# Performance work log

Hardware: AMD Instinct MI355X
Metric: run time of the kernel (lower is better)

The kernel has to match this reference:

```python
import jax, jax.numpy as jnp
import numpy as np

B, C, N, T = 16, 32, 1024, 64
C_OUT = 32
ORDER = 2
SMOOTH_DEPTH = 1


def setup_inputs() -> dict:
    key = jax.random.key(0)
    k1, k2, k3, k4 = jax.random.split(key, 4)
    x = jax.random.normal(k1, (B, C, N, T), dtype=jnp.float32)
    # row-normalized dense adjacencies (transition matrices), as used in Graph-WaveNet-style supports
    AL = jax.random.uniform(k2, (N, N), dtype=jnp.float32)
    AL = AL / AL.sum(axis=-1, keepdims=True)
    AS_pos = jax.random.uniform(k3, (N, N), dtype=jnp.float32)
    AS_pos = AS_pos / AS_pos.sum(axis=-1, keepdims=True)
    # 1x1 conv mlp: in_channels = (order*support_len+1)*c_in = 3*C, out_channels = C_OUT
    W_mlp = jax.random.normal(k4, (C_OUT, (ORDER + 1) * C), dtype=jnp.float32) * 0.02
    b_mlp = jnp.zeros((C_OUT,), dtype=jnp.float32)
    return {"x": x, "AL": AL, "AS_pos": AS_pos, "W_mlp": W_mlp, "b_mlp": b_mlp}


def reference(x, AL, AS_pos, W_mlp, b_mlp):
    # gcn_module.forward with short_bool=True, smooth_depth=SMOOTH_DEPTH, eval mode (no dropout)
    ALp = jnp.linalg.matrix_power(AL, SMOOTH_DEPTH)          # [N,N]
    # torch.einsum('bckj,ik->bcij', x, ALp): contract node dim of x against ALp
    x_long = jnp.einsum('ik,bckt->bcit', ALp, x)             # [B,C,N,T]
    x_short = x - x_long
    outs = [x]
    for _ in range(ORDER):
        # dnconv: einsum('nvw,ncwl->ncvl', A, x) with 2D A broadcast over batch
        x_long = jnp.einsum('vw,bcwt->bcvt', AL, x_long)
        x_short = jnp.einsum('vw,bcwt->bcvt', AS_pos, x_short)
        outs.append(x_long + x_short)
    h = jnp.concatenate(outs, axis=1)                        # [B,(ORDER+1)*C,N,T]
    # 1x1 conv == channel mixing
    h = jnp.einsum('oc,bcnt->bont', W_mlp, h) + b_mlp[None, :, None, None]
    return h
```

## Files before the change

### kernel.cpp

```cpp
#include <hip/hip_runtime.h>


typedef __bf16 bf16x8 __attribute__((ext_vector_type(8)));
typedef float f32x4 __attribute__((ext_vector_type(4)));
typedef unsigned int u32x4 __attribute__((ext_vector_type(4)));
typedef unsigned int u32x2 __attribute__((ext_vector_type(2)));

__device__ __forceinline__ unsigned short f2bf(float f) {
  unsigned u = __builtin_bit_cast(unsigned, f);
  u += 0x7fffu + ((u >> 16) & 1u);
  return (unsigned short)(u >> 16);
}
__device__ __forceinline__ float bf2f(unsigned short h) {
  unsigned u = ((unsigned)h) << 16;
  return __builtin_bit_cast(float, u);
}

static constexpr size_t OFF_YC    = 0;
static constexpr size_t OFF_ALBF  = 201326592;
static constexpr size_t OFF_ALT   = OFF_ALBF  + 2097152;
static constexpr size_t OFF_ASBF  = OFF_ALT   + 2097152;
static constexpr size_t OFF_AST   = OFF_ASBF  + 2097152;
static constexpr size_t OFF_AL2   = OFF_AST   + 2097152;
static constexpr size_t OFF_AL2T  = OFF_AL2   + 2097152;
static constexpr size_t OFF_ASAL  = OFF_AL2T  + 2097152;
static constexpr size_t OFF_AS2   = OFF_ASAL  + 2097152;
static constexpr size_t OFF_AL3   = OFF_AS2   + 2097152;
static constexpr size_t OFF_AS2AL = OFF_AL3   + 2097152;
static constexpr size_t OFF_G     = OFF_AS2AL + 2097152;

__global__ __launch_bounds__(256) void k_cast_bf16(const float* __restrict__ src,
                                                   unsigned short* __restrict__ dst,
                                                   int n4) {
  int i = blockIdx.x * 256 + threadIdx.x;
  if (i < n4) {
    float4 v = *((const float4*)src + i);
    unsigned lo = (unsigned)f2bf(v.x) | ((unsigned)f2bf(v.y) << 16);
    unsigned hi = (unsigned)f2bf(v.z) | ((unsigned)f2bf(v.w) << 16);
    u32x2 pk = {lo, hi};
    *(u32x2*)(dst + (size_t)i * 4) = pk;
  }
}

__global__ __launch_bounds__(256) void k_cast_wall(const float* __restrict__ W,
                                                   unsigned short* __restrict__ Wall) {
  int i = blockIdx.x * 256 + threadIdx.x;
  if (i < 3072) {
    int oo = i >> 5, c = i & 31;
    int o = oo & 31, g = oo >> 5;
    Wall[i] = f2bf(W[o * 96 + g * 32 + c]);
  }
}

__global__ __launch_bounds__(256) void k_transpose_cast(const float* __restrict__ src,
                                                        unsigned short* __restrict__ dst,
                                                        int R, int Cc) {
  __shared__ float Xs[64][65];
  const int tid = threadIdx.x;
  const size_t slice = (size_t)blockIdx.z * (size_t)R * (size_t)Cc;
  const float* s = src + slice;
  unsigned short* d = dst + slice;
  const int r0 = blockIdx.x * 64, c0 = blockIdx.y * 64;
  const int lrow = tid >> 4, lc4 = tid & 15;
#pragma unroll
  for (int rr = 0; rr < 4; rr++) {
    int row = rr * 16 + lrow;
    float4 v = *(const float4*)(s + (size_t)(r0 + row) * Cc + c0 + lc4 * 4);
    Xs[row][lc4 * 4 + 0] = v.x;
    Xs[row][lc4 * 4 + 1] = v.y;
    Xs[row][lc4 * 4 + 2] = v.z;
    Xs[row][lc4 * 4 + 3] = v.w;
  }
  __syncthreads();
  const int wc = tid & 7;
#pragma unroll
  for (int u = 0; u < 2; u++) {
    int t = u * 32 + (tid >> 3);
    unsigned v0 = (unsigned)f2bf(Xs[wc * 8 + 0][t]) | ((unsigned)f2bf(Xs[wc * 8 + 1][t]) << 16);
    unsigned v1 = (unsigned)f2bf(Xs[wc * 8 + 2][t]) | ((unsigned)f2bf(Xs[wc * 8 + 3][t]) << 16);
    unsigned v2 = (unsigned)f2bf(Xs[wc * 8 + 4][t]) | ((unsigned)f2bf(Xs[wc * 8 + 5][t]) << 16);
    unsigned v3 = (unsigned)f2bf(Xs[wc * 8 + 6][t]) | ((unsigned)f2bf(Xs[wc * 8 + 7][t]) << 16);
    u32x4 pk = {v0, v1, v2, v3};
    *(u32x4*)(d + (size_t)(c0 + t) * R + r0 + wc * 8) = pk;
  }
}

__device__ __forceinline__ void gemm128_bt(const unsigned short* __restrict__ A,
                                           const unsigned short* __restrict__ Bt,
                                           unsigned short* __restrict__ Cp,
                                           int K, size_t ldc, int m0, int n0) {
  __shared__ unsigned short As[128 * 32];
  __shared__ unsigned short Bs[128 * 32];
  const int tid = threadIdx.x;
  const int wave = tid >> 6, lane = tid & 63;
  const int lane15 = lane & 15, quad = lane >> 4;
  const int wm = wave & 1, wn = wave >> 1;
  const int srow = lane >> 2;
  const int schunk = (lane & 3) * 8;

  const unsigned short* gA0 = A + (size_t)(m0 + wave * 16 + srow) * K + schunk;
  const unsigned short* gA1 = A + (size_t)(m0 + 64 + wave * 16 + srow) * K + schunk;
  const unsigned short* gB0 = Bt + (size_t)(n0 + wave * 16 + srow) * K + schunk;
  const unsigned short* gB1 = Bt + (size_t)(n0 + 64 + wave * 16 + srow) * K + schunk;
  unsigned short* lA0 = As + (wave * 16) * 32;
  unsigned short* lA1 = As + (64 + wave * 16) * 32;
  unsigned short* lB0 = Bs + (wave * 16) * 32;
  unsigned short* lB1 = Bs + (64 + wave * 16) * 32;

  f32x4 acc[4][4];
#pragma unroll
  for (int i = 0; i < 4; i++)
#pragma unroll
    for (int j = 0; j < 4; j++) acc[i][j] = (f32x4){0.f, 0.f, 0.f, 0.f};

  const unsigned short* pa = As + (wm * 64 + lane15) * 32 + quad * 8;
  const unsigned short* pb = Bs + (wn * 64 + lane15) * 32 + quad * 8;

  for (int kb = 0; kb < K; kb += 32) {
    __syncthreads();
    __builtin_amdgcn_global_load_lds(
        (const __attribute__((address_space(1))) unsigned int*)(gA0 + kb),
        (__attribute__((address_space(3))) unsigned int*)lA0, 16, 0, 0);
    __builtin_amdgcn_global_load_lds(
        (const __attribute__((address_space(1))) unsigned int*)(gA1 + kb),
        (__attribute__((address_space(3))) unsigned int*)lA1, 16, 0, 0);
    __builtin_amdgcn_global_load_lds(
        (const __attribute__((address_space(1))) unsigned int*)(gB0 + kb),
        (__attribute__((address_space(3))) unsigned int*)lB0, 16, 0, 0);
    __builtin_amdgcn_global_load_lds(
        (const __attribute__((address_space(1))) unsigned int*)(gB1 + kb),
        (__attribute__((address_space(3))) unsigned int*)lB1, 16, 0, 0);
    __syncthreads();

    bf16x8 av[4], bv[4];
#pragma unroll
    for (int mt = 0; mt < 4; mt++) av[mt] = *(const bf16x8*)(pa + mt * 16 * 32);
#pragma unroll
    for (int nt = 0; nt < 4; nt++) bv[nt] = *(const bf16x8*)(pb + nt * 16 * 32);
#pragma unroll
    for (int mt = 0; mt < 4; mt++)
#pragma unroll
      for (int nt = 0; nt < 4; nt++)
        acc[mt][nt] = __builtin_amdgcn_mfma_f32_16x16x32_bf16(av[mt], bv[nt], acc[mt][nt], 0, 0, 0);
  }

#pragma unroll
  for (int mt = 0; mt < 4; mt++) {
#pragma unroll
    for (int nt = 0; nt < 4; nt++) {
      const int col = n0 + wn * 64 + nt * 16 + lane15;
#pragma unroll
      for (int r = 0; r < 4; r++) {
        const int row = m0 + wm * 64 + mt * 16 + quad * 4 + r;
        Cp[(size_t)row * ldc + col] = f2bf(acc[mt][nt][r]);
      }
    }
  }
}

__global__ __launch_bounds__(256) void k_gemm_pre(char* ws, int stage) {
  const unsigned short* A;
  const unsigned short* Bt;
  unsigned short* Cp;
  const int z = blockIdx.z;
  unsigned short* ALbf = (unsigned short*)(ws + OFF_ALBF);
  unsigned short* ALt  = (unsigned short*)(ws + OFF_ALT);
  unsigned short* ASbf = (unsigned short*)(ws + OFF_ASBF);
  unsigned short* ASt  = (unsigned short*)(ws + OFF_AST);
  unsigned short* AL2  = (unsigned short*)(ws + OFF_AL2);
  unsigned short* ASAL = (unsigned short*)(ws + OFF_ASAL);
  unsigned short* AS2  = (unsigned short*)(ws + OFF_AS2);
  unsigned short* AL3  = (unsigned short*)(ws + OFF_AL3);
  unsigned short* AS2AL= (unsigned short*)(ws + OFF_AS2AL);
  if (stage == 0) {
    if (z == 0)      { A = ALbf; Bt = ALt;  Cp = AL2;  }
    else if (z == 1) { A = ASbf; Bt = ALt;  Cp = ASAL; }
    else             { A = ASbf; Bt = ASt;  Cp = AS2;  }
  } else {
    if (z == 0)      { A = AL2;  Bt = ALt;  Cp = AL3;  }
    else             { A = AS2;  Bt = ALt;  Cp = AS2AL;}
  }
  gemm128_bt(A, Bt, Cp, 1024, 1024, blockIdx.y * 128, blockIdx.x * 128);
}

__global__ __launch_bounds__(256) void k_assemble_G(const unsigned short* __restrict__ AL2,
                                                    const unsigned short* __restrict__ ASAL,
                                                    const float* __restrict__ ASf,
                                                    const unsigned short* __restrict__ AL3,
                                                    const unsigned short* __restrict__ AS2,
                                                    const unsigned short* __restrict__ AS2AL,
                                                    unsigned short* __restrict__ G) {
  int i = blockIdx.x * 256 + threadIdx.x;
  int r = i >> 10, c = i & 1023;
  float g1 = bf2f(AL2[i]) + ASf[i] - bf2f(ASAL[i]);
  float g2 = bf2f(AL3[i]) + bf2f(AS2[i]) - bf2f(AS2AL[i]);
  G[(size_t)r * 2048 + c]        = f2bf(g1);
  G[(size_t)r * 2048 + 1024 + c] = f2bf(g2);
}

__global__ __launch_bounds__(256, 8) void k_mix_g(const float* __restrict__ x,
                                                  const unsigned short* __restrict__ Wall,
                                                  unsigned short* __restrict__ Yc) {
  const int tid = threadIdx.x;
  const int sid = (blockIdx.x & 7) * 256 + (blockIdx.x >> 3);
  const int b   = sid >> 7;
  const int n8g = sid & 127;
  const int nbase = n8g * 8;
  const int wave = tid >> 6, lane = tid & 63;
  const int lane15 = lane & 15, quad = lane >> 4;
  const int t = wave * 16 + lane15;

  bf16x8 afr[6];
#pragma unroll
  for (int ot = 0; ot < 6; ot++)
    afr[ot] = *(const bf16x8*)(Wall + (ot * 16 + lane15) * 32 + quad * 8);

  const float* xb = x + (size_t)b * 2097152 + (size_t)(quad * 8) * 65536 + t;

  bf16x8 bfr[8];
#pragma unroll
  for (int nl = 0; nl < 8; nl++) {
    const float* xp = xb + (size_t)(nbase + nl) * 64;
    unsigned u[4];
#pragma unroll
    for (int e = 0; e < 4; e++) {
      float a  = xp[(size_t)(2 * e) * 65536];
      float c2 = xp[(size_t)(2 * e + 1) * 65536];
      u[e] = (unsigned)f2bf(a) | ((unsigned)f2bf(c2) << 16);
    }
    u32x4 pk = {u[0], u[1], u[2], u[3]};
    bfr[nl] = __builtin_bit_cast(bf16x8, pk);
  }

#pragma unroll
  for (int ot = 0; ot < 6; ot++) {
    f32x4 acc[8];
    const f32x4 z = (f32x4){0.f, 0.f, 0.f, 0.f};
#pragma unroll
    for (int nl = 0; nl < 8; nl++)
      acc[nl] = __builtin_amdgcn_mfma_f32_16x16x32_bf16(afr[ot], bfr[nl], z, 0, 0, 0);
    const int og = ot >> 1;
    const int o  = (ot & 1) * 16 + quad * 4;
    const size_t plane = (size_t)(og * 128 + n8g) * 262144;
#pragma unroll
    for (int r = 0; r < 4; r++) {
      unsigned u0 = (unsigned)f2bf(acc[0][r]) | ((unsigned)f2bf(acc[1][r]) << 16);
      unsigned u1 = (unsigned)f2bf(acc[2][r]) | ((unsigned)f2bf(acc[3][r]) << 16);
      unsigned u2 = (unsigned)f2bf(acc[4][r]) | ((unsigned)f2bf(acc[5][r]) << 16);
      unsigned u3 = (unsigned)f2bf(acc[6][r]) | ((unsigned)f2bf(acc[7][r]) << 16);
      u32x4 pk = {u0, u1, u2, u3};
      size_t j = (size_t)(b * 32 + o + r) * 64 + t;
      *(u32x4*)(Yc + plane + j * 8) = pk;
    }
  }
}

__global__ __launch_bounds__(512) void k_gemm_main8(const unsigned short* __restrict__ A,
                                                    const unsigned short* __restrict__ Yc,
                                                    const float* __restrict__ bm,
                                                    float* __restrict__ out) {
  __shared__ unsigned short lds[65536];
  const int tid = threadIdx.x;
  const int wave = tid >> 6, lane = tid & 63;
  const int lane15 = lane & 15, quad = lane >> 4;
  const int wr = wave >> 2, wc = wave & 3;

  const int bid = blockIdx.x;
  const int swz = (bid & 7) * 64 + (bid >> 3);
  const int nx = swz >> 2, my = swz & 3;
  const int m0 = my * 256, n0 = nx * 256;

  const int srow = tid >> 3;
  const int cB   = (tid & 7) ^ (srow & 7);
  const int skc  = cB << 3;
  const int ldst0 = (tid & ~63) << 3;

#define STAGE_A(rowbase, ldsptr, ktile)                                                 \
  do {                                                                                  \
    const unsigned short* _g =                                                          \
        A + (size_t)((rowbase) + srow) * 2048 + (size_t)((ktile) * 64 + skc);           \
    __builtin_amdgcn_global_load_lds(                                                   \
        (const __attribute__((address_space(1))) unsigned int*)_g,                      \
        (__attribute__((address_space(3))) unsigned int*)((ldsptr) + ldst0), 16, 0, 0); \
    __builtin_amdgcn_global_load_lds(                                                   \
        (const __attribute__((address_space(1))) unsigned int*)(_g + 131072),           \
        (__attribute__((address_space(3))) unsigned int*)((ldsptr) + 4096 + ldst0),     \
        16, 0, 0);                                                                      \
  } while (0)

#define STAGE_B(rowbase, ldsptr, ktile)                                                 \
  do {                                                                                  \
    const unsigned short* _g = Yc + (size_t)(128 + (ktile) * 8 + cB) * 262144 +         \
                               (size_t)((rowbase) + srow) * 8;                          \
    __builtin_amdgcn_global_load_lds(                                                   \
        (const __attribute__((address_space(1))) unsigned int*)_g,                      \
        (__attribute__((address_space(3))) unsigned int*)((ldsptr) + ldst0), 16, 0, 0); \
    __builtin_amdgcn_global_load_lds(                                                   \
        (const __attribute__((address_space(1))) unsigned int*)(_g + 512),              \
        (__attribute__((address_space(3))) unsigned int*)((ldsptr) + 4096 + ldst0),     \
        16, 0, 0);                                                                      \
  } while (0)

#define LOAD_AFR(p)                                                                     \
  bf16x8 afr[2][2];                                                                     \
  _Pragma("unroll") for (int mi = 0; mi < 2; mi++)                                      \
      _Pragma("unroll") for (int kk = 0; kk < 2; kk++)                                  \
          afr[mi][kk] = *(const bf16x8*)(pA + (2 * (p) + mi) * 1024 + aks[kk]);

#define MFMA_QUAD(p)                                                                    \
  _Pragma("unroll") for (int kk = 0; kk < 2; kk++)                                      \
      _Pragma("unroll") for (int mi = 0; mi < 2; mi++)                                  \
          _Pragma("unroll") for (int n = 0; n < 4; n++)                                 \
              acc[2 * (p) + mi][n] = __builtin_amdgcn_mfma_f32_16x16x32_bf16(           \
                  afr[mi][kk], bfr[n][kk], acc[2 * (p) + mi][n], 0, 0, 0);

#define PHASE_SYNC_PRE()                              \
  asm volatile("" ::: "memory");                      \
  __builtin_amdgcn_s_barrier();                       \
  asm volatile("s_waitcnt lgkmcnt(0)" ::: "memory");  \
  __builtin_amdgcn_sched_barrier(0);                  \
  __builtin_amdgcn_s_setprio(1);

#define PHASE_SYNC_POST()                             \
  __builtin_amdgcn_s_setprio(0);                      \
  asm volatile("" ::: "memory");                      \
  __builtin_amdgcn_s_barrier();

  unsigned short* Acur = lds;
  unsigned short* Bcur = lds + 16384;
  unsigned short* Aalt = lds + 32768;
  unsigned short* Balt = lds + 49152;

  f32x4 acc[8][4];
#pragma unroll
  for (int i = 0; i < 8; i++)
#pragma unroll
    for (int j = 0; j < 4; j++) acc[i][j] = (f32x4){0.f, 0.f, 0.f, 0.f};

  const int swz8 = (lane15 & 7) << 3;
  int aks[2];
  aks[0] = (quad << 3) ^ swz8;
  aks[1] = (32 | (quad << 3)) ^ swz8;

  STAGE_B(n0,       Bcur,        0);
  STAGE_B(n0 + 128, Bcur + 8192, 0);
  STAGE_A(m0,       Acur,        0);
  STAGE_A(m0 + 128, Acur + 8192, 0);
  STAGE_B(n0,       Balt,        1);
  STAGE_B(n0 + 128, Balt + 8192, 1);
  STAGE_A(m0,       Aalt,        1);
  asm volatile("s_waitcnt vmcnt(6)" ::: "memory");
  __builtin_amdgcn_s_barrier();

  for (int u = 0; u < 30; ++u) {
    const unsigned short* pA = Acur + (wr * 128 + lane15) * 64;
    const unsigned short* pB = Bcur + (wc * 64 + lane15) * 64;
    bf16x8 bfr[4][2];
    {
#pragma unroll
      for (int n = 0; n < 4; n++)
#pragma unroll
        for (int kk = 0; kk < 2; kk++)
          bfr[n][kk] = *(const bf16x8*)(pB + n * 1024 + aks[kk]);
      LOAD_AFR(0)
      __builtin_amdgcn_sched_barrier(0);
      STAGE_A(m0 + 128, Aalt + 8192, u + 1);
      asm volatile("s_waitcnt lgkmcnt(8)" ::: "memory");
      PHASE_SYNC_PRE()
      MFMA_QUAD(0)
      PHASE_SYNC_POST()
    }
    {
      LOAD_AFR(1)
      __builtin_amdgcn_sched_barrier(0);
      STAGE_B(n0, Bcur, u + 2);
      PHASE_SYNC_PRE()
      MFMA_QUAD(1)
      PHASE_SYNC_POST()
    }
    {
      LOAD_AFR(2)
      __builtin_amdgcn_sched_barrier(0);
      STAGE_B(n0 + 128, Bcur + 8192, u + 2);
      PHASE_SYNC_PRE()
      MFMA_QUAD(2)
      PHASE_SYNC_POST()
    }
    {
      LOAD_AFR(3)
      __builtin_amdgcn_sched_barrier(0);
      STAGE_A(m0, Acur, u + 2);
      PHASE_SYNC_PRE()
      MFMA_QUAD(3)
      __builtin_amdgcn_s_setprio(0);
      asm volatile("s_waitcnt vmcnt(6)" ::: "memory");
      asm volatile("" ::: "memory");
      __builtin_amdgcn_s_barrier();
    }
    unsigned short* t;
    t = Acur; Acur = Aalt; Aalt = t;
    t = Bcur; Bcur = Balt; Balt = t;
  }

  {
    const unsigned short* pA = Acur + (wr * 128 + lane15) * 64;
    const unsigned short* pB = Bcur + (wc * 64 + lane15) * 64;
    bf16x8 bfr[4][2];
    {
#pragma unroll
      for (int n = 0; n < 4; n++)
#pragma unroll
        for (int kk = 0; kk < 2; kk++)
          bfr[n][kk] = *(const bf16x8*)(pB + n * 1024 + aks[kk]);
      LOAD_AFR(0)
      __builtin_amdgcn_sched_barrier(0);
      STAGE_A(m0 + 128, Aalt + 8192, 31);
      asm volatile("s_waitcnt lgkmcnt(8)" ::: "memory");
      PHASE_SYNC_PRE()
      MFMA_QUAD(0)
      PHASE_SYNC_POST()
    }
    { LOAD_AFR(1) PHASE_SYNC_PRE() MFMA_QUAD(1) PHASE_SYNC_POST() }
    { LOAD_AFR(2) PHASE_SYNC_PRE() MFMA_QUAD(2) PHASE_SYNC_POST() }
    {
      LOAD_AFR(3)
      PHASE_SYNC_PRE()
      MFMA_QUAD(3)
      __builtin_amdgcn_s_setprio(0);
      asm volatile("s_waitcnt vmcnt(0)" ::: "memory");
      asm volatile("" ::: "memory");
      __builtin_amdgcn_s_barrier();
    }
    unsigned short* t;
    t = Acur; Acur = Aalt; Aalt = t;
    t = Bcur; Bcur = Balt; Balt = t;
  }

  {
    const unsigned short* pA = Acur + (wr * 128 + lane15) * 64;
    const unsigned short* pB = Bcur + (wc * 64 + lane15) * 64;
    bf16x8 bfr[4][2];
#pragma unroll
    for (int n = 0; n < 4; n++)
#pragma unroll
      for (int kk = 0; kk < 2; kk++)
        bfr[n][kk] = *(const bf16x8*)(pB + n * 1024 + aks[kk]);
#pragma unroll
    for (int p = 0; p < 4; p++) {
      bf16x8 afr[2][2];
#pragma unroll
      for (int mi = 0; mi < 2; mi++)
#pragma unroll
        for (int kk = 0; kk < 2; kk++)
          afr[mi][kk] = *(const bf16x8*)(pA + (2 * p + mi) * 1024 + aks[kk]);
#pragma unroll
      for (int kk = 0; kk < 2; kk++)
#pragma unroll
        for (int mi = 0; mi < 2; mi++)
#pragma unroll
          for (int n = 0; n < 4; n++)
            acc[2 * p + mi][n] = __builtin_amdgcn_mfma_f32_16x16x32_bf16(
                afr[mi][kk], bfr[n][kk], acc[2 * p + mi][n], 0, 0, 0);
    }
  }

#pragma unroll
  for (int mt = 0; mt < 8; mt++) {
    const int row = m0 + wr * 128 + mt * 16 + quad * 4;
#pragma unroll
    for (int nf = 0; nf < 4; nf++) {
      const int col = n0 + wc * 64 + nf * 16 + lane15;
      const int bo_idx = col >> 6;
      const float bo = bm[bo_idx & 31];
      const size_t obase = (size_t)bo_idx * 65536 + (col & 63);
      ushort4 yv = *(const ushort4*)(Yc + (size_t)(row >> 3) * 262144 +
                                     (size_t)col * 8 + (row & 7));
      out[obase + (size_t)(row + 0) * 64] = acc[mt][nf][0] + bf2f(yv.x) + bo;
      out[obase + (size_t)(row + 1) * 64] = acc[mt][nf][1] + bf2f(yv.y) + bo;
      out[obase + (size_t)(row + 2) * 64] = acc[mt][nf][2] + bf2f(yv.z) + bo;
      out[obase + (size_t)(row + 3) * 64] = acc[mt][nf][3] + bf2f(yv.w) + bo;
    }
  }
#undef STAGE_A
#undef STAGE_B
#undef LOAD_AFR
#undef MFMA_QUAD
#undef PHASE_SYNC_PRE
#undef PHASE_SYNC_POST
}

extern "C" void kernel_launch(void* const* d_in, const int* in_sizes, int n_in,
                              void* d_out, int out_size, void* d_ws, size_t ws_size,
                              hipStream_t stream) {
  const float* x  = (const float*)d_in[0];
  const float* AL = (const float*)d_in[1];
  const float* AS = (const float*)d_in[2];
  const float* W  = (const float*)d_in[3];
  const float* bm = (const float*)d_in[4];
  float* out = (float*)d_out;
  char* ws = (char*)d_ws;

  unsigned short* Yc    = (unsigned short*)(ws + OFF_YC);
  unsigned short* ALbf  = (unsigned short*)(ws + OFF_ALBF);
  unsigned short* ALt   = (unsigned short*)(ws + OFF_ALT);
  unsigned short* ASbf  = (unsigned short*)(ws + OFF_ASBF);
  unsigned short* ASt   = (unsigned short*)(ws + OFF_AST);
  unsigned short* AL2   = (unsigned short*)(ws + OFF_AL2);
  unsigned short* ASAL  = (unsigned short*)(ws + OFF_ASAL);
  unsigned short* AS2   = (unsigned short*)(ws + OFF_AS2);
  unsigned short* AL3   = (unsigned short*)(ws + OFF_AL3);
  unsigned short* AS2AL = (unsigned short*)(ws + OFF_AS2AL);
  unsigned short* Gm    = (unsigned short*)(ws + OFF_G);
  unsigned short* Wall  = (unsigned short*)(ws + OFF_ALBF);

  k_cast_bf16<<<1024, 256, 0, stream>>>(AL, ALbf, 262144);
  k_cast_bf16<<<1024, 256, 0, stream>>>(AS, ASbf, 262144);
  k_transpose_cast<<<dim3(16, 16, 1), 256, 0, stream>>>(AL, ALt, 1024, 1024);
  k_transpose_cast<<<dim3(16, 16, 1), 256, 0, stream>>>(AS, ASt, 1024, 1024);
  k_gemm_pre<<<dim3(8, 8, 3), 256, 0, stream>>>(ws, 0);
  k_gemm_pre<<<dim3(8, 8, 2), 256, 0, stream>>>(ws, 1);
  k_assemble_G<<<4096, 256, 0, stream>>>(AL2, ASAL, AS, AL3, AS2, AS2AL, Gm);
  k_cast_wall<<<12, 256, 0, stream>>>(W, Wall);
  k_mix_g<<<2048, 256, 0, stream>>>(x, Wall, Yc);
  k_gemm_main8<<<dim3(512, 1, 1), 512, 0, stream>>>(Gm, Yc, bm, out);
}
```

Measured before the change: 519.1 us.

## Fuse adjacency prep kernels and re-pipeline main GEMM with ping-pong A fragments

The bf16 cast and transpose-cast of each adjacency become one k_prep kernel, which reads each source tile once and writes both layouts. The W cast is folded into block 0 of k_assemble_G, removing two launches. The main GEMM loop is restructured so that A fragments alternate between two register sets (afrP and afrQ): the next fragment's LDS reads and the async global-to-LDS stage are issued before a barrier, ahead of the current MFMA group. The loop-head barrier is moved and the vmcnt wait is loosened from 6 to 4. These changes aim to overlap LDS reads with MFMAs and reduce launch overhead, at the cost of more live registers and a subtler LDS hazard ordering.

```diff
diff --git a/kernel.cpp b/kernel.cpp
--- a/kernel.cpp
+++ b/kernel.cpp
@@ -29,47 +29,25 @@
 static constexpr size_t OFF_AS2AL = OFF_AL3   + 2097152;
 static constexpr size_t OFF_G     = OFF_AS2AL + 2097152;
 
-__global__ __launch_bounds__(256) void k_cast_bf16(const float* __restrict__ src,
-                                                   unsigned short* __restrict__ dst,
-                                                   int n4) {
-  int i = blockIdx.x * 256 + threadIdx.x;
-  if (i < n4) {
-    float4 v = *((const float4*)src + i);
-    unsigned lo = (unsigned)f2bf(v.x) | ((unsigned)f2bf(v.y) << 16);
-    unsigned hi = (unsigned)f2bf(v.z) | ((unsigned)f2bf(v.w) << 16);
-    u32x2 pk = {lo, hi};
-    *(u32x2*)(dst + (size_t)i * 4) = pk;
-  }
-}
-
-__global__ __launch_bounds__(256) void k_cast_wall(const float* __restrict__ W,
-                                                   unsigned short* __restrict__ Wall) {
-  int i = blockIdx.x * 256 + threadIdx.x;
-  if (i < 3072) {
-    int oo = i >> 5, c = i & 31;
-    int o = oo & 31, g = oo >> 5;
-    Wall[i] = f2bf(W[o * 96 + g * 32 + c]);
-  }
-}
-
-__global__ __launch_bounds__(256) void k_transpose_cast(const float* __restrict__ src,
-                                                        unsigned short* __restrict__ dst,
-                                                        int R, int Cc) {
+__global__ __launch_bounds__(256) void k_prep(const float* __restrict__ src,
+                                              unsigned short* __restrict__ dstN,
+                                              unsigned short* __restrict__ dstT) {
   __shared__ float Xs[64][65];
   const int tid = threadIdx.x;
-  const size_t slice = (size_t)blockIdx.z * (size_t)R * (size_t)Cc;
-  const float* s = src + slice;
-  unsigned short* d = dst + slice;
   const int r0 = blockIdx.x * 64, c0 = blockIdx.y * 64;
   const int lrow = tid >> 4, lc4 = tid & 15;
 #pragma unroll
   for (int rr = 0; rr < 4; rr++) {
     int row = rr * 16 + lrow;
-    float4 v = *(const float4*)(s + (size_t)(r0 + row) * Cc + c0 + lc4 * 4);
+    float4 v = *(const float4*)(src + (size_t)(r0 + row) * 1024 + c0 + lc4 * 4);
     Xs[row][lc4 * 4 + 0] = v.x;
     Xs[row][lc4 * 4 + 1] = v.y;
     Xs[row][lc4 * 4 + 2] = v.z;
     Xs[row][lc4 * 4 + 3] = v.w;
+    unsigned lo = (unsigned)f2bf(v.x) | ((unsigned)f2bf(v.y) << 16);
+    unsigned hi = (unsigned)f2bf(v.z) | ((unsigned)f2bf(v.w) << 16);
+    u32x2 pk = {lo, hi};
+    *(u32x2*)(dstN + (size_t)(r0 + row) * 1024 + c0 + lc4 * 4) = pk;
   }
   __syncthreads();
   const int wc = tid & 7;
@@ -81,7 +59,7 @@
     unsigned v2 = (unsigned)f2bf(Xs[wc * 8 + 4][t]) | ((unsigned)f2bf(Xs[wc * 8 + 5][t]) << 16);
     unsigned v3 = (unsigned)f2bf(Xs[wc * 8 + 6][t]) | ((unsigned)f2bf(Xs[wc * 8 + 7][t]) << 16);
     u32x4 pk = {v0, v1, v2, v3};
-    *(u32x4*)(d + (size_t)(c0 + t) * R + r0 + wc * 8) = pk;
+    *(u32x4*)(dstT + (size_t)(c0 + t) * 1024 + r0 + wc * 8) = pk;
   }
 }
 
@@ -189,7 +167,15 @@
                                                     const unsigned short* __restrict__ AL3,
                                                     const unsigned short* __restrict__ AS2,
                                                     const unsigned short* __restrict__ AS2AL,
+                                                    const float* __restrict__ W,
+                                                    unsigned short* __restrict__ Wall,
                                                     unsigned short* __restrict__ G) {
+  if (blockIdx.x == 0) {
+    for (int k = threadIdx.x; k < 3072; k += 256) {
+      int oo = k >> 5, c = k & 31;
+      Wall[k] = f2bf(W[(oo & 31) * 96 + (oo >> 5) * 32 + c]);
+    }
+  }
   int i = blockIdx.x * 256 + threadIdx.x;
   int r = i >> 10, c = i & 1023;
   float g1 = bf2f(AL2[i]) + ASf[i] - bf2f(ASAL[i]);
@@ -301,30 +287,31 @@
         16, 0, 0);                                                                      \
   } while (0)
 
-#define LOAD_AFR(p)                                                                     \
-  bf16x8 afr[2][2];                                                                     \
-  _Pragma("unroll") for (int mi = 0; mi < 2; mi++)                                      \
+#define RD_BFR()                                                                        \
+  _Pragma("unroll") for (int n = 0; n < 4; n++)                                         \
       _Pragma("unroll") for (int kk = 0; kk < 2; kk++)                                  \
-          afr[mi][kk] = *(const bf16x8*)(pA + (2 * (p) + mi) * 1024 + aks[kk]);
-
-#define MFMA_QUAD(p)                                                                    \
+          bfr[n][kk] = *(const bf16x8*)(pB + n * 1024 + aks[kk]);
+
+#define RD_AFR(FR, mA, mB)                                                              \
+  _Pragma("unroll") for (int kk = 0; kk < 2; kk++) {                                    \
+    FR[0][kk] = *(const bf16x8*)(pA + (mA) * 1024 + aks[kk]);                           \
+    FR[1][kk] = *(const bf16x8*)(pA + (mB) * 1024 + aks[kk]);                           \
+  }
+
+#define MFMA2(i0, FR)                                                                   \
   _Pragma("unroll") for (int kk = 0; kk < 2; kk++)                                      \
       _Pragma("unroll") for (int mi = 0; mi < 2; mi++)                                  \
           _Pragma("unroll") for (int n = 0; n < 4; n++)                                 \
-              acc[2 * (p) + mi][n] = __builtin_amdgcn_mfma_f32_16x16x32_bf16(           \
-                  afr[mi][kk], bfr[n][kk], acc[2 * (p) + mi][n], 0, 0, 0);
-
-#define PHASE_SYNC_PRE()                              \
-  asm volatile("" ::: "memory");                      \
-  __builtin_amdgcn_s_barrier();                       \
-  asm volatile("s_waitcnt lgkmcnt(0)" ::: "memory");  \
-  __builtin_amdgcn_sched_barrier(0);                  \
-  __builtin_amdgcn_s_setprio(1);
-
-#define PHASE_SYNC_POST()                             \
-  __builtin_amdgcn_s_setprio(0);                      \
-  asm volatile("" ::: "memory");                      \
+              acc[(i0) + mi][n] = __builtin_amdgcn_mfma_f32_16x16x32_bf16(              \
+                  FR[mi][kk], bfr[n][kk], acc[(i0) + mi][n], 0, 0, 0);
+
+#define SAFEBAR()                                                                       \
+  asm volatile("s_waitcnt lgkmcnt(0)" ::: "memory");                                    \
   __builtin_amdgcn_s_barrier();
+#define LGKM0() asm volatile("s_waitcnt lgkmcnt(0)" ::: "memory");                      \
+                __builtin_amdgcn_sched_barrier(0);
+#define PRIO1() __builtin_amdgcn_s_setprio(1);
+#define PRIO0() __builtin_amdgcn_s_setprio(0);
 
   unsigned short* Acur = lds;
   unsigned short* Bcur = lds + 16384;
@@ -341,6 +328,8 @@
   int aks[2];
   aks[0] = (quad << 3) ^ swz8;
   aks[1] = (32 | (quad << 3)) ^ swz8;
+
+  bf16x8 bfr[4][2], afrP[2][2], afrQ[2][2];
 
   STAGE_B(n0,       Bcur,        0);
   STAGE_B(n0 + 128, Bcur + 8192, 0);
@@ -350,53 +339,32 @@
   STAGE_B(n0 + 128, Balt + 8192, 1);
   STAGE_A(m0,       Aalt,        1);
   asm volatile("s_waitcnt vmcnt(6)" ::: "memory");
-  __builtin_amdgcn_s_barrier();
 
   for (int u = 0; u < 30; ++u) {
     const unsigned short* pA = Acur + (wr * 128 + lane15) * 64;
     const unsigned short* pB = Bcur + (wc * 64 + lane15) * 64;
-    bf16x8 bfr[4][2];
-    {
-#pragma unroll
-      for (int n = 0; n < 4; n++)
-#pragma unroll
-        for (int kk = 0; kk < 2; kk++)
-          bfr[n][kk] = *(const bf16x8*)(pB + n * 1024 + aks[kk]);
-      LOAD_AFR(0)
-      __builtin_amdgcn_sched_barrier(0);
-      STAGE_A(m0 + 128, Aalt + 8192, u + 1);
-      asm volatile("s_waitcnt lgkmcnt(8)" ::: "memory");
-      PHASE_SYNC_PRE()
-      MFMA_QUAD(0)
-      PHASE_SYNC_POST()
-    }
-    {
-      LOAD_AFR(1)
-      __builtin_amdgcn_sched_barrier(0);
-      STAGE_B(n0, Bcur, u + 2);
-      PHASE_SYNC_PRE()
-      MFMA_QUAD(1)
-      PHASE_SYNC_POST()
-    }
-    {
-      LOAD_AFR(2)
-      __builtin_amdgcn_sched_barrier(0);
-      STAGE_B(n0 + 128, Bcur + 8192, u + 2);
-      PHASE_SYNC_PRE()
-      MFMA_QUAD(2)
-      PHASE_SYNC_POST()
-    }
-    {
-      LOAD_AFR(3)
-      __builtin_amdgcn_sched_barrier(0);
-      STAGE_A(m0, Acur, u + 2);
-      PHASE_SYNC_PRE()
-      MFMA_QUAD(3)
-      __builtin_amdgcn_s_setprio(0);
-      asm volatile("s_waitcnt vmcnt(6)" ::: "memory");
-      asm volatile("" ::: "memory");
-      __builtin_amdgcn_s_barrier();
-    }
+    SAFEBAR();
+    RD_BFR();
+    RD_AFR(afrP, 0, 1);
+    LGKM0();
+    PRIO1(); MFMA2(0, afrP); PRIO0();
+    RD_AFR(afrQ, 2, 3);
+    STAGE_A(m0 + 128, Aalt + 8192, u + 1);
+    SAFEBAR();
+    __builtin_amdgcn_sched_barrier(0);
+    PRIO1(); MFMA2(2, afrQ); PRIO0();
+    RD_AFR(afrP, 4, 5);
+    STAGE_B(n0, Bcur, u + 2);
+    SAFEBAR();
+    __builtin_amdgcn_sched_barrier(0);
+    PRIO1(); MFMA2(4, afrP); PRIO0();
+    RD_AFR(afrQ, 6, 7);
+    STAGE_B(n0 + 128, Bcur + 8192, u + 2);
+    SAFEBAR();
+    __builtin_amdgcn_sched_barrier(0);
+    PRIO1(); MFMA2(6, afrQ); PRIO0();
+    STAGE_A(m0, Acur, u + 2);
+    asm volatile("s_waitcnt vmcnt(4)" ::: "memory");
     unsigned short* t;
     t = Acur; Acur = Aalt; Aalt = t;
     t = Bcur; Bcur = Balt; Balt = t;
@@ -405,32 +373,26 @@
   {
     const unsigned short* pA = Acur + (wr * 128 + lane15) * 64;
     const unsigned short* pB = Bcur + (wc * 64 + lane15) * 64;
-    bf16x8 bfr[4][2];
-    {
-#pragma unroll
-      for (int n = 0; n < 4; n++)
-#pragma unroll
-        for (int kk = 0; kk < 2; kk++)
-          bfr[n][kk] = *(const bf16x8*)(pB + n * 1024 + aks[kk]);
-      LOAD_AFR(0)
-      __builtin_amdgcn_sched_barrier(0);
-      STAGE_A(m0 + 128, Aalt + 8192, 31);
-      asm volatile("s_waitcnt lgkmcnt(8)" ::: "memory");
-      PHASE_SYNC_PRE()
-      MFMA_QUAD(0)
-      PHASE_SYNC_POST()
-    }
-    { LOAD_AFR(1) PHASE_SYNC_PRE() MFMA_QUAD(1) PHASE_SYNC_POST() }
-    { LOAD_AFR(2) PHASE_SYNC_PRE() MFMA_QUAD(2) PHASE_SYNC_POST() }
-    {
-      LOAD_AFR(3)
-      PHASE_SYNC_PRE()
-      MFMA_QUAD(3)
-      __builtin_amdgcn_s_setprio(0);
-      asm volatile("s_waitcnt vmcnt(0)" ::: "memory");
-      asm volatile("" ::: "memory");
-      __builtin_amdgcn_s_barrier();
-    }
+    SAFEBAR();
+    RD_BFR();
+    RD_AFR(afrP, 0, 1);
+    LGKM0();
+    PRIO1(); MFMA2(0, afrP); PRIO0();
+    RD_AFR(afrQ, 2, 3);
+    STAGE_A(m0 + 128, Aalt + 8192, 31);
+    SAFEBAR();
+    __builtin_amdgcn_sched_barrier(0);
+    PRIO1(); MFMA2(2, afrQ); PRIO0();
+    RD_AFR(afrP, 4, 5);
+    SAFEBAR();
+    __builtin_amdgcn_sched_barrier(0);
+    PRIO1(); MFMA2(4, afrP); PRIO0();
+    RD_AFR(afrQ, 6, 7);
+    SAFEBAR();
+    __builtin_amdgcn_sched_barrier(0);
+    PRIO1(); MFMA2(6, afrQ); PRIO0();
+    asm volatile("s_waitcnt vmcnt(0)" ::: "memory");
+    SAFEBAR();
     unsigned short* t;
     t = Acur; Acur = Aalt; Aalt = t;
     t = Bcur; Bcur = Balt; Balt = t;
@@ -439,12 +401,7 @@
   {
     const unsigned short* pA = Acur + (wr * 128 + lane15) * 64;
     const unsigned short* pB = Bcur + (wc * 64 + lane15) * 64;
-    bf16x8 bfr[4][2];
-#pragma unroll
-    for (int n = 0; n < 4; n++)
-#pragma unroll
-      for (int kk = 0; kk < 2; kk++)
-        bfr[n][kk] = *(const bf16x8*)(pB + n * 1024 + aks[kk]);
+    RD_BFR();
 #pragma unroll
     for (int p = 0; p < 4; p++) {
       bf16x8 afr[2][2];
@@ -483,10 +440,13 @@
   }
 #undef STAGE_A
 #undef STAGE_B
-#undef LOAD_AFR
-#undef MFMA_QUAD
-#undef PHASE_SYNC_PRE
-#undef PHASE_SYNC_POST
+#undef RD_BFR
+#undef RD_AFR
+#undef MFMA2
+#undef SAFEBAR
+#undef LGKM0
+#undef PRIO1
+#undef PRIO0
 }
 
 extern "C" void kernel_launch(void* const* d_in, const int* in_sizes, int n_in,
@@ -513,14 +473,11 @@
   unsigned short* Gm    = (unsigned short*)(ws + OFF_G);
   unsigned short* Wall  = (unsigned short*)(ws + OFF_ALBF);
 
-  k_cast_bf16<<<1024, 256, 0, stream>>>(AL, ALbf, 262144);
-  k_cast_bf16<<<1024, 256, 0, stream>>>(AS, ASbf, 262144);
-  k_transpose_cast<<<dim3(16, 16, 1), 256, 0, stream>>>(AL, ALt, 1024, 1024);
-  k_transpose_cast<<<dim3(16, 16, 1), 256, 0, stream>>>(AS, ASt, 1024, 1024);
+  k_prep<<<dim3(16, 16, 1), 256, 0, stream>>>(AL, ALbf, ALt);
+  k_prep<<<dim3(16, 16, 1), 256, 0, stream>>>(AS, ASbf, ASt);
   k_gemm_pre<<<dim3(8, 8, 3), 256, 0, stream>>>(ws, 0);
   k_gemm_pre<<<dim3(8, 8, 2), 256, 0, stream>>>(ws, 1);
-  k_assemble_G<<<4096, 256, 0, stream>>>(AL2, ASAL, AS, AL3, AS2, AS2AL, Gm);
-  k_cast_wall<<<12, 256, 0, stream>>>(W, Wall);
+  k_assemble_G<<<4096, 256, 0, stream>>>(AL2, ASAL, AS, AL3, AS2, AS2AL, W, Wall, Gm);
   k_mix_g<<<2048, 256, 0, stream>>>(x, Wall, Yc);
   k_gemm_main8<<<dim3(512, 1, 1), 512, 0, stream>>>(Gm, Yc, bm, out);
 }
```

Result: no change. 518.0 us (-0.2%).
